# Performance work log

Hardware: AMD Instinct MI355X
Metric: run time of the kernel (lower is better)

## Reference

```python
import jax, jax.numpy as jnp
import numpy as np

B, S, D, H = 2, 2048, 1024, 16
DK = D // H


def setup_inputs() -> dict:
    key = jax.random.key(0)
    ks = jax.random.split(key, 12)
    std = 1.0 / np.sqrt(D)
    inp = {
        "query": jax.random.normal(ks[0], (B, S, D), jnp.float32),
        "key": jax.random.normal(ks[1], (B, S, D), jnp.float32),
        "value": jax.random.normal(ks[2], (B, S, D), jnp.float32),
        # causal decoder mask [B, 1, S, S]; 0 -> masked
        "mask": jnp.broadcast_to(jnp.tril(jnp.ones((S, S), jnp.int32)), (B, 1, S, S)),
        "wq": jax.random.uniform(ks[3], (D, D), jnp.float32, -std, std),
        "bq": jax.random.uniform(ks[4], (D,), jnp.float32, -std, std),
        "wk": jax.random.uniform(ks[5], (D, D), jnp.float32, -std, std),
        "bk": jax.random.uniform(ks[6], (D,), jnp.float32, -std, std),
        "wv": jax.random.uniform(ks[7], (D, D), jnp.float32, -std, std),
        "bv": jax.random.uniform(ks[8], (D,), jnp.float32, -std, std),
        "wo": jax.random.uniform(ks[9], (D, D), jnp.float32, -std, std),
        "bo": jax.random.uniform(ks[10], (D,), jnp.float32, -std, std),
    }
    return inp


def _split_heads(x):
    b, s, _ = x.shape
    return x.reshape(b, s, H, DK).transpose(0, 2, 1, 3)  # [B,H,S,DK]


def reference(query, key, value, mask, wq, bq, wk, bk, wv, bv, wo, bo):
    # nn.Linear: y = x @ W^T + b
    q = _split_heads(query @ wq.T + bq)
    k = _split_heads(key @ wk.T + bk)
    v = _split_heads(value @ wv.T + bv)
    scores = jnp.einsum("bhqd,bhkd->bhqk", q, k) / np.sqrt(DK).astype(np.float32)
    scores = jnp.where(mask == 0, jnp.float32(-1e9), scores)
    attn = jax.nn.softmax(scores, axis=-1)
    # dropout is identity in eval mode
    out = jnp.einsum("bhqk,bhkd->bhqd", attn, v)
    out = out.transpose(0, 2, 1, 3).reshape(query.shape[0], -1, D)
    return out @ wo.T + bo
```

## Files before the change

kernel.cpp:

```cpp
#include <hip/hip_runtime.h>
#include <hip/hip_bf16.h>
#include <cstdint>
#include <cstddef>

#define B_ 2
#define S_ 2048
#define D_ 1024
#define H_ 16
#define DK_ 64

#define AS1 __attribute__((address_space(1)))
#define AS3 __attribute__((address_space(3)))

typedef __attribute__((ext_vector_type(8))) short short8;
typedef __attribute__((ext_vector_type(4))) float f32x4;
typedef __attribute__((ext_vector_type(16))) float f32x16;
typedef __attribute__((ext_vector_type(4))) unsigned short ushort4_t;

__device__ __forceinline__ unsigned short f2bf(float f) {
    union { float f; unsigned u; } x; x.f = f;
    unsigned r = x.u + 0x7fffu + ((x.u >> 16) & 1u);
    return (unsigned short)(r >> 16);
}

__device__ __forceinline__ unsigned pack_bf16(float lo, float hi_) {
    union { __hip_bfloat162 h; unsigned u; } cv;
    cv.h = __float22bfloat162_rn(make_float2(lo, hi_));
    return cv.u;
}

__device__ __forceinline__ float xor32f(float x, int hi) {
#if __has_builtin(__builtin_amdgcn_permlane32_swap)
    unsigned u = __builtin_bit_cast(unsigned, x);
    auto r = __builtin_amdgcn_permlane32_swap(u, u, false, false);
    return __builtin_bit_cast(float, hi ? r[0] : r[1]);
#else
    return __shfl_xor(x, 32);
#endif
}

__device__ __forceinline__ void swap32(unsigned a, unsigned b, unsigned& x, unsigned& y, int hi) {
#if __has_builtin(__builtin_amdgcn_permlane32_swap)
    auto r = __builtin_amdgcn_permlane32_swap(a, b, false, false);
    x = r[0]; y = r[1];
#else
    unsigned pa_ = __shfl_xor(a, 32), pb_ = __shfl_xor(b, 32);
    x = hi ? pb_ : a;
    y = hi ? b : pa_;
#endif
}

__global__ __launch_bounds__(256) void cvt_all(
    const float* __restrict__ q, const float* __restrict__ k, const float* __restrict__ v,
    const float* __restrict__ wq, const float* __restrict__ wk, const float* __restrict__ wv,
    const float* __restrict__ wo,
    unsigned short* __restrict__ xq, unsigned short* __restrict__ xk, unsigned short* __restrict__ xv,
    unsigned short* __restrict__ wqb, unsigned short* __restrict__ wkb, unsigned short* __restrict__ wvb,
    unsigned short* __restrict__ wob) {
    int b = blockIdx.x;
    const float* src; unsigned short* dst; int rel;
    if (b < 6144) {
        int which = b >> 11; rel = b & 2047;
        src = (which == 0) ? q : (which == 1) ? k : v;
        dst = (which == 0) ? xq : (which == 1) ? xk : xv;
    } else {
        int bb = b - 6144; int which = bb >> 9; rel = bb & 511;
        src = (which == 0) ? wq : (which == 1) ? wk : (which == 2) ? wv : wo;
        dst = (which == 0) ? wqb : (which == 1) ? wkb : (which == 2) ? wvb : wob;
    }
    int i = rel * 256 + threadIdx.x;
    const float4* s4 = (const float4*)src;
    float4 a = s4[2 * i], c = s4[2 * i + 1];
    short8 o;
    o[0] = (short)f2bf(a.x); o[1] = (short)f2bf(a.y); o[2] = (short)f2bf(a.z); o[3] = (short)f2bf(a.w);
    o[4] = (short)f2bf(c.x); o[5] = (short)f2bf(c.y); o[6] = (short)f2bf(c.z); o[7] = (short)f2bf(c.w);
    *(short8*)(dst + (size_t)i * 8) = o;
}

template <int OUTMODE>
__device__ __forceinline__ void gemm_body(const unsigned short* __restrict__ A,
                                          const unsigned short* __restrict__ W,
                                          const float* __restrict__ bias,
                                          void* __restrict__ Cout, float scale) {
    constexpr int Kd = 1024;
    __shared__ unsigned short As[128 * 64];
    __shared__ unsigned short Bs[128 * 64];
    const int t = threadIdx.x;
    const int l = t & 63;
    const int l15 = l & 15, l4 = l >> 4;
    const int wid = t >> 6;
    const int wm = wid >> 1, wn = wid & 1;
    const int m0 = (blockIdx.x * 4 + (blockIdx.y & 3)) * 128;
    const int n0 = (blockIdx.y >> 2) * 128;

    f32x4 acc[4][4] = {};

    int ldsoff[4];
    size_t sgoff[4];
#pragma unroll
    for (int p = 0; p < 4; p++) {
        int off = p * 4096 + t * 16;
        int row = off >> 7;
        int slot = (off >> 4) & 7;
        ldsoff[p] = off;
        sgoff[p] = (size_t)row * Kd + (size_t)((slot ^ (row & 7)) * 8);
    }

    for (int k0 = 0; k0 < Kd; k0 += 64) {
#pragma unroll
        for (int p = 0; p < 4; p++)
            __builtin_amdgcn_global_load_lds(
                (const AS1 void*)(A + (size_t)m0 * Kd + sgoff[p] + k0),
                (AS3 void*)((char*)As + ldsoff[p]), 16, 0, 0);
#pragma unroll
        for (int p = 0; p < 4; p++)
            __builtin_amdgcn_global_load_lds(
                (const AS1 void*)(W + (size_t)n0 * Kd + sgoff[p] + k0),
                (AS3 void*)((char*)Bs + ldsoff[p]), 16, 0, 0);
        __syncthreads();
#pragma unroll
        for (int kk = 0; kk < 2; kk++) {
            short8 af[4], bfr[4];
#pragma unroll
            for (int mi = 0; mi < 4; mi++) {
                int row = wm * 64 + mi * 16 + l15;
                int slot = kk * 4 + l4;
                af[mi] = *(const short8*)((const char*)As + row * 128 + ((slot ^ (row & 7)) << 4));
            }
#pragma unroll
            for (int ni = 0; ni < 4; ni++) {
                int row = wn * 64 + ni * 16 + l15;
                int slot = kk * 4 + l4;
                bfr[ni] = *(const short8*)((const char*)Bs + row * 128 + ((slot ^ (row & 7)) << 4));
            }
#pragma unroll
            for (int mi = 0; mi < 4; mi++)
#pragma unroll
                for (int ni = 0; ni < 4; ni++)
                    acc[mi][ni] = __builtin_amdgcn_mfma_f32_16x16x32_bf16(af[mi], bfr[ni], acc[mi][ni], 0, 0, 0);
        }
        __syncthreads();
    }

#pragma unroll
    for (int mi = 0; mi < 4; mi++) {
#pragma unroll
        for (int ni = 0; ni < 4; ni++) {
            int n = n0 + wn * 64 + ni * 16 + l15;
            float bn = bias[n];
            int mb = m0 + wm * 64 + mi * 16 + l4 * 4;
            if constexpr (OUTMODE == 2) {
                int b = mb >> 11, s = mb & 2047, h = n >> 6, dk = n & 63;
                ushort4_t vv;
#pragma unroll
                for (int j = 0; j < 4; j++) vv[j] = f2bf(acc[mi][ni][j] + bn);
                *(ushort4_t*)((unsigned short*)Cout + ((size_t)(b * H_ + h) * DK_ + dk) * S_ + s) = vv;
            } else {
#pragma unroll
                for (int j = 0; j < 4; j++) {
                    float v = (acc[mi][ni][j] + bn) * scale;
                    int m = mb + j;
                    if constexpr (OUTMODE == 0) {
                        int b = m >> 11, s = m & 2047, h = n >> 6, dk = n & 63;
                        ((unsigned short*)Cout)[(((size_t)b * H_ + h) * S_ + s) * DK_ + dk] = f2bf(v);
                    } else {
                        ((float*)Cout)[(size_t)m * D_ + n] = v;
                    }
                }
            }
        }
    }
}

__global__ __launch_bounds__(256) void qkv_gemm(
    const unsigned short* __restrict__ xq, const unsigned short* __restrict__ xk,
    const unsigned short* __restrict__ xv, const unsigned short* __restrict__ wqb,
    const unsigned short* __restrict__ wkb, const unsigned short* __restrict__ wvb,
    const float* __restrict__ bq, const float* __restrict__ bk, const float* __restrict__ bv,
    unsigned short* __restrict__ qo, unsigned short* __restrict__ ko, unsigned short* __restrict__ vto,
    float qscale) {
    int z = blockIdx.z;
    if (z == 2) {
        gemm_body<2>(xv, wvb, bv, vto, 1.0f);
    } else {
        const unsigned short* A = (z == 0) ? xq : xk;
        const unsigned short* W = (z == 0) ? wqb : wkb;
        const float* bias = (z == 0) ? bq : bk;
        unsigned short* out = (z == 0) ? qo : ko;
        float scale = (z == 0) ? qscale : 1.0f;
        gemm_body<0>(A, W, bias, out, scale);
    }
}

__global__ __launch_bounds__(256) void out_gemm(const unsigned short* __restrict__ Aa,
                                                const unsigned short* __restrict__ Wo,
                                                const float* __restrict__ bo,
                                                float* __restrict__ out) {
    gemm_body<1>(Aa, Wo, bo, out, 1.0f);
}

__device__ __forceinline__ void attn_compute(const short8 kf[4], const short8 vf[4],
                                             const short8 qf[4], int lq, int hi, bool diag,
                                             f32x16& o0, f32x16& o1, float& l_run) {
    f32x16 sT = {};
    __builtin_amdgcn_s_setprio(1);
#pragma unroll
    for (int c = 0; c < 4; c++)
        sT = __builtin_amdgcn_mfma_f32_32x32x16_bf16(kf[c], qf[c], sT, 0, 0, 0);
    __builtin_amdgcn_s_setprio(0);

    float e[16];
#pragma unroll
    for (int r = 0; r < 16; r++) e[r] = exp2f(sT[r]);
    if (diag) {
#pragma unroll
        for (int r = 0; r < 16; r++) {
            int kvl = (r & 3) + 8 * (r >> 2) + 4 * hi;
            e[r] = (kvl <= lq) ? e[r] : 0.0f;
        }
    }

    float s8[8];
#pragma unroll
    for (int r = 0; r < 8; r++) s8[r] = e[2 * r] + e[2 * r + 1];
#pragma unroll
    for (int r = 0; r < 4; r++) s8[r] = s8[r] + s8[r + 4];
    float ps = (s8[0] + s8[1]) + (s8[2] + s8[3]);
    ps += xor32f(ps, hi);
    l_run += ps;

    unsigned OW[8];
#pragma unroll
    for (int w = 0; w < 8; w++) OW[w] = pack_bf16(e[2 * w], e[2 * w + 1]);

    union { unsigned u[4]; short8 s; } pa0, pa1;
    swap32(OW[0], OW[2], pa0.u[0], pa0.u[2], hi);
    swap32(OW[1], OW[3], pa0.u[1], pa0.u[3], hi);
    swap32(OW[4], OW[6], pa1.u[0], pa1.u[2], hi);
    swap32(OW[5], OW[7], pa1.u[1], pa1.u[3], hi);

    __builtin_amdgcn_s_setprio(1);
    o0 = __builtin_amdgcn_mfma_f32_32x32x16_bf16(pa0.s, vf[0], o0, 0, 0, 0);
    o1 = __builtin_amdgcn_mfma_f32_32x32x16_bf16(pa0.s, vf[1], o1, 0, 0, 0);
    o0 = __builtin_amdgcn_mfma_f32_32x32x16_bf16(pa1.s, vf[2], o0, 0, 0, 0);
    o1 = __builtin_amdgcn_mfma_f32_32x32x16_bf16(pa1.s, vf[3], o1, 0, 0, 0);
    __builtin_amdgcn_s_setprio(0);
}

__global__ __launch_bounds__(512, 4) void attn_kernel(const unsigned short* __restrict__ Q,
                                                      const unsigned short* __restrict__ Kk,
                                                      const unsigned short* __restrict__ Vt,
                                                      unsigned short* __restrict__ Aout) {
    __shared__ union SM {
        unsigned short kv[2][2][128 * 64];
        struct { float obuf[2][2][32][64]; float lArr[2][4][32]; } m;
    } sm;

    const int t_ = threadIdx.x;
    const int l = t_ & 63;
    const int w = t_ >> 6;
    const int qsub = w >> 2, kvw = w & 3;
    const int lq = l & 31, hi = l >> 5;

    const int bid = blockIdx.x;
    const int xcd = bid & 7, j = bid >> 3;
    const int bh = xcd * 4 + (j >> 5);
    const int bq = 31 - (j & 31);
    const int wq0 = bq * 64;
    const int qi = 2 * bq + qsub;
    const int T = ((2 * bq + 1) >> 2) + 1;

    const unsigned short* Qh = Q + (size_t)bh * S_ * DK_;
    const unsigned short* Kh = Kk + (size_t)bh * S_ * DK_;
    const unsigned short* Vth = Vt + (size_t)bh * DK_ * S_;

    short8 qf[4];
    const unsigned short* qrow = Qh + (size_t)(wq0 + qsub * 32 + lq) * DK_ + hi * 8;
#pragma unroll
    for (int c = 0; c < 4; c++) qf[c] = *(const short8*)(qrow + 16 * c);

    f32x16 o0 = {}, o1 = {};
    float l_run = 0.f;

#define STAGE_TILE(BUF, TILE)                                                                \
    {                                                                                        \
        const char* Kb = (const char*)Kh + (size_t)(TILE)*16384;                             \
        _Pragma("unroll") for (int p = 0; p < 2; p++) {                                      \
            int off = p * 8192 + t_ * 16;                                                    \
            int r = off >> 7, sl = (off >> 4) & 7;                                           \
            __builtin_amdgcn_global_load_lds(                                                \
                (const AS1 void*)(Kb + r * 128 + ((sl ^ (r & 7)) << 4)),                     \
                (AS3 void*)((char*)sm.kv[BUF][0] + off), 16, 0, 0);                          \
        }                                                                                    \
        const char* Vb = (const char*)Vth + (size_t)(TILE)*256;                              \
        _Pragma("unroll") for (int p = 0; p < 2; p++) {                                      \
            int off = p * 8192 + t_ * 16;                                                    \
            int r = off >> 8, sl = (off >> 4) & 15;                                          \
            __builtin_amdgcn_global_load_lds(                                                \
                (const AS1 void*)(Vb + (size_t)r * (S_ * 2) + ((sl ^ (r & 15)) << 4)),       \
                (AS3 void*)((char*)sm.kv[BUF][1] + off), 16, 0, 0);                          \
        }                                                                                    \
    }

    STAGE_TILE(0, 0);
    STAGE_TILE(1, 1);

    for (int t = 0; t < T; t++) {
        if (t + 1 < T) { asm volatile("s_waitcnt vmcnt(4)" ::: "memory"); }
        else           { asm volatile("s_waitcnt vmcnt(0)" ::: "memory"); }
        __builtin_amdgcn_sched_barrier(0);
        __builtin_amdgcn_s_barrier();
        __builtin_amdgcn_sched_barrier(0);

        const int sidx = 4 * t + kvw;
        if (sidx <= qi) {
            short8 kf[4], vf[4];
            const int lr = kvw * 32 + lq;
            const char* Kbuf = (const char*)sm.kv[t & 1][0];
            const char* Vbuf = (const char*)sm.kv[t & 1][1];
#pragma unroll
            for (int c = 0; c < 4; c++)
                kf[c] = *(const short8*)(Kbuf + lr * 128 + (((2 * c + hi) ^ (lr & 7)) << 4));
#pragma unroll
            for (int c = 0; c < 2; c++) {
                int slot = kvw * 4 + 2 * c + hi;
                vf[2 * c] = *(const short8*)(Vbuf + lq * 256 + ((slot ^ (lq & 15)) << 4));
                int r1 = lq + 32;
                vf[2 * c + 1] = *(const short8*)(Vbuf + r1 * 256 + ((slot ^ (r1 & 15)) << 4));
            }
            attn_compute(kf, vf, qf, lq, hi, sidx == qi, o0, o1, l_run);
        }

        asm volatile("s_waitcnt lgkmcnt(0)" ::: "memory");
        __builtin_amdgcn_sched_barrier(0);
        __builtin_amdgcn_s_barrier();
        __builtin_amdgcn_sched_barrier(0);

        if (t + 2 < T) STAGE_TILE(t & 1, t + 2);
    }

    float(&obuf)[2][2][32][64] = sm.m.obuf;
    float(&lArr)[2][4][32] = sm.m.lArr;
    if (hi == 0) lArr[qsub][kvw][lq] = l_run;

    if (kvw < 2) {
#pragma unroll
        for (int r = 0; r < 16; r++) {
            int qrw = (r & 3) + 8 * (r >> 2) + 4 * hi;
            obuf[qsub][kvw][qrw][lq] = o0[r];
            obuf[qsub][kvw][qrw][lq + 32] = o1[r];
        }
    }
    __syncthreads();
    if (kvw >= 2) {
#pragma unroll
        for (int r = 0; r < 16; r++) {
            int qrw = (r & 3) + 8 * (r >> 2) + 4 * hi;
            obuf[qsub][kvw - 2][qrw][lq] += o0[r];
            obuf[qsub][kvw - 2][qrw][lq + 32] += o1[r];
        }
    }
    __syncthreads();

    const int b = bh >> 4, h = bh & 15;
    const int row = (w & 3) * 8 + (l >> 3);
    const int dk0 = (l & 7) * 8;
    float ls = lArr[qsub][0][row] + lArr[qsub][1][row] + lArr[qsub][2][row] + lArr[qsub][3][row];
    float inv = 1.0f / ls;
    short8 ov;
#pragma unroll
    for (int jj = 0; jj < 8; jj++) {
        float s = obuf[qsub][0][row][dk0 + jj] + obuf[qsub][1][row][dk0 + jj];
        ov[jj] = (short)f2bf(s * inv);
    }
    unsigned short* orow = Aout + ((size_t)b * S_ + (wq0 + qsub * 32 + row)) * D_ + h * 64 + dk0;
    *(short8*)orow = ov;
}

extern "C" void kernel_launch(void* const* d_in, const int* in_sizes, int n_in,
                              void* d_out, int out_size, void* d_ws, size_t ws_size,
                              hipStream_t stream) {
    const float* query = (const float*)d_in[0];
    const float* key = (const float*)d_in[1];
    const float* value = (const float*)d_in[2];
    const float* wq = (const float*)d_in[4];
    const float* bq = (const float*)d_in[5];
    const float* wk = (const float*)d_in[6];
    const float* bk = (const float*)d_in[7];
    const float* wv = (const float*)d_in[8];
    const float* bv = (const float*)d_in[9];
    const float* wo = (const float*)d_in[10];
    const float* bo = (const float*)d_in[11];

    const size_t NX = (size_t)B_ * S_ * D_;
    const size_t NW = (size_t)D_ * D_;
    char* p = (char*)d_ws;
    unsigned short* xq = (unsigned short*)p; p += NX * 2;
    unsigned short* xk = (unsigned short*)p; p += NX * 2;
    unsigned short* xv = (unsigned short*)p; p += NX * 2;
    unsigned short* wqb = (unsigned short*)p; p += NW * 2;
    unsigned short* wkb = (unsigned short*)p; p += NW * 2;
    unsigned short* wvb = (unsigned short*)p; p += NW * 2;
    unsigned short* wob = (unsigned short*)p; p += NW * 2;
    unsigned short* qb = (unsigned short*)p; p += NX * 2;
    unsigned short* kb = (unsigned short*)p; p += NX * 2;
    unsigned short* vtb = (unsigned short*)p; p += NX * 2;
    unsigned short* ab = (unsigned short*)p; p += NX * 2;

    cvt_all<<<dim3(8192), dim3(256), 0, stream>>>(query, key, value, wq, wk, wv, wo,
                                                  xq, xk, xv, wqb, wkb, wvb, wob);

    const float qscale = 0.125f * 1.4426950408889634f;
    qkv_gemm<<<dim3(8, 32, 3), dim3(256), 0, stream>>>(xq, xk, xv, wqb, wkb, wvb,
                                                       bq, bk, bv, qb, kb, vtb, qscale);
    attn_kernel<<<dim3(1024), dim3(512), 0, stream>>>(qb, kb, vtb, ab);
    out_gemm<<<dim3(8, 32), dim3(256), 0, stream>>>(ab, wob, bo, (float*)d_out);
}
```

Baseline: 129.6 us.

## Load K/V fragments directly from global memory, dropping LDS double-buffer staging

Replaces the LDS double-buffered K/V staging (global_load_lds with swizzle, barriers and waitcnt) with per-wave direct global loads of the K and V^T fragments into registers. Each wave now walks its own KV chunks independently without block-wide barriers. This removes the synchronization and LDS traffic and shrinks shared memory, but loses the cross-wave sharing of staged tiles. It also loses the prefetch overlap, so each wave waits on global/L2 latency right before its MFMAs.

```diff
diff --git a/kernel.cpp b/kernel.cpp
--- a/kernel.cpp
+++ b/kernel.cpp
@@ -251,10 +251,7 @@
                                                       const unsigned short* __restrict__ Kk,
                                                       const unsigned short* __restrict__ Vt,
                                                       unsigned short* __restrict__ Aout) {
-    __shared__ union SM {
-        unsigned short kv[2][2][128 * 64];
-        struct { float obuf[2][2][32][64]; float lArr[2][4][32]; } m;
-    } sm;
+    __shared__ struct { float obuf[2][2][32][64]; float lArr[2][4][32]; } sm;
 
     const int t_ = threadIdx.x;
     const int l = t_ & 63;
@@ -268,7 +265,6 @@
     const int bq = 31 - (j & 31);
     const int wq0 = bq * 64;
     const int qi = 2 * bq + qsub;
-    const int T = ((2 * bq + 1) >> 2) + 1;
 
     const unsigned short* Qh = Q + (size_t)bh * S_ * DK_;
     const unsigned short* Kh = Kk + (size_t)bh * S_ * DK_;
@@ -282,65 +278,27 @@
     f32x16 o0 = {}, o1 = {};
     float l_run = 0.f;
 
-#define STAGE_TILE(BUF, TILE)                                                                \
-    {                                                                                        \
-        const char* Kb = (const char*)Kh + (size_t)(TILE)*16384;                             \
-        _Pragma("unroll") for (int p = 0; p < 2; p++) {                                      \
-            int off = p * 8192 + t_ * 16;                                                    \
-            int r = off >> 7, sl = (off >> 4) & 7;                                           \
-            __builtin_amdgcn_global_load_lds(                                                \
-                (const AS1 void*)(Kb + r * 128 + ((sl ^ (r & 7)) << 4)),                     \
-                (AS3 void*)((char*)sm.kv[BUF][0] + off), 16, 0, 0);                          \
-        }                                                                                    \
-        const char* Vb = (const char*)Vth + (size_t)(TILE)*256;                              \
-        _Pragma("unroll") for (int p = 0; p < 2; p++) {                                      \
-            int off = p * 8192 + t_ * 16;                                                    \
-            int r = off >> 8, sl = (off >> 4) & 15;                                          \
-            __builtin_amdgcn_global_load_lds(                                                \
-                (const AS1 void*)(Vb + (size_t)r * (S_ * 2) + ((sl ^ (r & 15)) << 4)),       \
-                (AS3 void*)((char*)sm.kv[BUF][1] + off), 16, 0, 0);                          \
-        }                                                                                    \
-    }
-
-    STAGE_TILE(0, 0);
-    STAGE_TILE(1, 1);
-
-    for (int t = 0; t < T; t++) {
-        if (t + 1 < T) { asm volatile("s_waitcnt vmcnt(4)" ::: "memory"); }
-        else           { asm volatile("s_waitcnt vmcnt(0)" ::: "memory"); }
-        __builtin_amdgcn_sched_barrier(0);
-        __builtin_amdgcn_s_barrier();
-        __builtin_amdgcn_sched_barrier(0);
-
-        const int sidx = 4 * t + kvw;
-        if (sidx <= qi) {
-            short8 kf[4], vf[4];
-            const int lr = kvw * 32 + lq;
-            const char* Kbuf = (const char*)sm.kv[t & 1][0];
-            const char* Vbuf = (const char*)sm.kv[t & 1][1];
-#pragma unroll
-            for (int c = 0; c < 4; c++)
-                kf[c] = *(const short8*)(Kbuf + lr * 128 + (((2 * c + hi) ^ (lr & 7)) << 4));
-#pragma unroll
-            for (int c = 0; c < 2; c++) {
-                int slot = kvw * 4 + 2 * c + hi;
-                vf[2 * c] = *(const short8*)(Vbuf + lq * 256 + ((slot ^ (lq & 15)) << 4));
-                int r1 = lq + 32;
-                vf[2 * c + 1] = *(const short8*)(Vbuf + r1 * 256 + ((slot ^ (r1 & 15)) << 4));
-            }
-            attn_compute(kf, vf, qf, lq, hi, sidx == qi, o0, o1, l_run);
-        }
-
-        asm volatile("s_waitcnt lgkmcnt(0)" ::: "memory");
-        __builtin_amdgcn_sched_barrier(0);
-        __builtin_amdgcn_s_barrier();
-        __builtin_amdgcn_sched_barrier(0);
-
-        if (t + 2 < T) STAGE_TILE(t & 1, t + 2);
-    }
-
-    float(&obuf)[2][2][32][64] = sm.m.obuf;
-    float(&lArr)[2][4][32] = sm.m.lArr;
+    const unsigned short* kp  = Kh  + ((size_t)kvw * 32 + lq) * DK_ + hi * 8;
+    const unsigned short* vp0 = Vth + (size_t)lq * S_ + kvw * 32 + hi * 8;
+    const unsigned short* vp1 = vp0 + (size_t)32 * S_;
+
+    for (int sc = kvw; sc <= qi; sc += 4) {
+        short8 kf[4], vf[4];
+#pragma unroll
+        for (int c = 0; c < 4; c++) kf[c] = *(const short8*)(kp + 16 * c);
+#pragma unroll
+        for (int c = 0; c < 2; c++) {
+            vf[2 * c]     = *(const short8*)(vp0 + 16 * c);
+            vf[2 * c + 1] = *(const short8*)(vp1 + 16 * c);
+        }
+        attn_compute(kf, vf, qf, lq, hi, sc == qi, o0, o1, l_run);
+        kp  += 4 * 32 * DK_;
+        vp0 += 4 * 32;
+        vp1 += 4 * 32;
+    }
+
+    float(&obuf)[2][2][32][64] = sm.obuf;
+    float(&lArr)[2][4][32] = sm.lArr;
     if (hi == 0) lArr[qsub][kvw][lq] = l_run;
 
     if (kvw < 2) {
```

After: 167.2 us. 29.0% more time.
